# Kernel tuning notes

Measured on AMD Instinct MI355X. Metric: run time of the kernel, lower is better.

The kernel has to match this reference:

```python
import jax, jax.numpy as jnp
import numpy as np
import math

B = 256      # graphs per batch
NPG = 400    # nodes per graph (initial)
DEG = 16     # avg degree
F_IN = 128
H = 128
C = 2
NL = 5       # num_layers
RATIO = 0.8


def setup_inputs() -> dict:
    key = jax.random.key(0)
    ks = jax.random.split(key, 12)
    N = B * NPG
    E = B * NPG * DEG
    x = jax.random.normal(ks[0], (N, F_IN), dtype=jnp.float32)
    gid = jnp.repeat(jnp.arange(B, dtype=jnp.int32), NPG * DEG)
    src = jax.random.randint(ks[1], (E,), 0, NPG, dtype=jnp.int32) + gid * NPG
    dst = jax.random.randint(ks[2], (E,), 0, NPG, dtype=jnp.int32) + gid * NPG
    edge_index = jnp.stack([src, dst])
    batch = jnp.repeat(jnp.arange(B, dtype=jnp.int32), NPG)
    s = 0.05
    return dict(
        x=x, edge_index=edge_index, batch=batch,
        conv1_wr=jax.random.normal(ks[3], (F_IN, H), jnp.float32) * s,
        conv1_ws=jax.random.normal(ks[4], (F_IN, H), jnp.float32) * s,
        conv1_b=jnp.zeros((H,), jnp.float32),
        convs_wr=jax.random.normal(ks[5], (NL - 1, H, H), jnp.float32) * s,
        convs_ws=jax.random.normal(ks[6], (NL - 1, H, H), jnp.float32) * s,
        convs_b=jnp.zeros((NL - 1, H), jnp.float32),
        pools_wr=jax.random.normal(ks[7], ((NL - 1) // 2, H, 1), jnp.float32) * s,
        pools_ws=jax.random.normal(ks[8], ((NL - 1) // 2, H, 1), jnp.float32) * s,
        pools_b=jnp.zeros(((NL - 1) // 2, 1), jnp.float32),
        lin1_w=jax.random.normal(ks[9], (NL * H, H), jnp.float32) * s,
        lin1_b=jnp.zeros((H,), jnp.float32),
        lin2_w=jax.random.normal(ks[10], (H, C), jnp.float32) * s,
        lin2_b=jnp.zeros((C,), jnp.float32),
    )


def _graph_conv(x, src, dst, emask, n, wr, ws, b):
    # PyG GraphConv(aggr='mean'): mean_j(x_j) @ W_rel + x @ W_root + b
    msg = x[src] * emask[:, None]                       # [E, F]
    agg = jax.ops.segment_sum(msg, dst, num_segments=n)  # [N, F]
    cnt = jax.ops.segment_sum(emask, dst, num_segments=n)
    mean = agg / jnp.maximum(cnt, 1.0)[:, None]
    return mean @ wr + x @ ws + b


def _sag_pool(x, src, dst, emask, n, npg, wr, ws, b):
    # score via GraphConv(hidden, 1); per-graph top-k (fixed k since graphs equal-sized)
    score = _graph_conv(x, src, dst, emask, n, wr, ws, b)[:, 0]  # [N]
    nb = n // npg
    k = int(math.ceil(RATIO * npg))
    _, topi = jax.lax.top_k(score.reshape(nb, npg), k)           # [nb, k]
    perm = (topi + (jnp.arange(nb, dtype=topi.dtype) * npg)[:, None]).reshape(-1)
    new_x = x[perm] * jnp.tanh(score[perm])[:, None]
    # reindex edges; drop edges touching removed nodes via mask
    node_map = jnp.full((n,), -1, dtype=src.dtype).at[perm].set(
        jnp.arange(nb * k, dtype=src.dtype))
    ns, nd = node_map[src], node_map[dst]
    new_mask = emask * (ns >= 0).astype(emask.dtype) * (nd >= 0).astype(emask.dtype)
    return new_x, jnp.maximum(ns, 0), jnp.maximum(nd, 0), new_mask, nb * k, k


def reference(x, edge_index, batch, conv1_wr, conv1_ws, conv1_b,
              convs_wr, convs_ws, convs_b, pools_wr, pools_ws, pools_b,
              lin1_w, lin1_b, lin2_w, lin2_b):
    src, dst = edge_index[0], edge_index[1]
    emask = jnp.ones(src.shape, jnp.float32)
    n, npg = x.shape[0], NPG
    x = jax.nn.relu(_graph_conv(x, src, dst, emask, n, conv1_wr, conv1_ws, conv1_b))
    xs = [x.reshape(B, npg, H).mean(axis=1)]  # global_mean_pool (equal graph sizes)
    nconvs = NL - 1
    for i in range(nconvs):
        x = jax.nn.relu(_graph_conv(x, src, dst, emask, n,
                                    convs_wr[i], convs_ws[i], convs_b[i]))
        xs.append(x.reshape(B, npg, H).mean(axis=1))
        if i % 2 == 0 and i < nconvs - 1:
            j = i // 2
            x, src, dst, emask, n, npg = _sag_pool(
                x, src, dst, emask, n, npg, pools_wr[j], pools_ws[j], pools_b[j])
    h = jnp.concatenate(xs, axis=-1)            # JumpingKnowledge 'cat' -> [B, NL*H]
    h = jax.nn.relu(h @ lin1_w + lin1_b)        # dropout p=0.5 is identity (eval)
    logits = h @ lin2_w + lin2_b
    return jax.nn.log_softmax(logits, axis=-1)
```

## Files before the change

### kernel.cpp

```cpp
#include <hip/hip_runtime.h>
#include <math.h>

#define BGR 256
#define NPG0 400
#define NN (BGR*NPG0)
#define NE (NN*16)
#define HD 128
#define AST4 208
#define A32PG (NPG0*52)
#define KSA 13
#define MSTR 136
#define NTPB 5
#define SCGRID 2048
#define ACH4 1040

typedef __attribute__((ext_vector_type(8))) short short8;
typedef __attribute__((ext_vector_type(4))) float floatx4;
typedef __attribute__((ext_vector_type(4))) unsigned int uintx4;

__device__ __forceinline__ unsigned short f2b(float f) {
    unsigned int u = __builtin_bit_cast(unsigned int, f);
    unsigned int r = (u + 0x7fffu + ((u >> 16) & 1u)) >> 16;
    return (unsigned short)r;
}
__device__ __forceinline__ unsigned int pk2(float a, float b) {
    return (unsigned int)f2b(a) | ((unsigned int)f2b(b) << 16);
}
__device__ __forceinline__ float b2f_lo(unsigned int u) { return __builtin_bit_cast(float, u << 16); }
__device__ __forceinline__ float b2f_hi(unsigned int u) { return __builtin_bit_cast(float, u & 0xffff0000u); }
__device__ __forceinline__ short bfint(unsigned int v) {
    return (short)(__builtin_bit_cast(unsigned int, (float)v) >> 16);
}
__device__ __forceinline__ unsigned int pkb(short a, short b) {
    return (unsigned int)(unsigned short)a | ((unsigned int)(unsigned short)b << 16);
}
__device__ __forceinline__ short8 lutdec(unsigned int u, const unsigned int* lut) {
    uintx4 w;
    w[0] = lut[u & 0xFFu];
    w[1] = lut[(u >> 8) & 0xFFu];
    w[2] = lut[(u >> 16) & 0xFFu];
    w[3] = lut[u >> 24];
    return __builtin_bit_cast(short8, w);
}
__device__ __forceinline__ float nibdot(unsigned int u, const float* v) {
    return (float)(u & 0xFu) * v[0] + (float)((u >> 4) & 0xFu) * v[1]
         + (float)((u >> 8) & 0xFu) * v[2] + (float)((u >> 12) & 0xFu) * v[3]
         + (float)((u >> 16) & 0xFu) * v[4] + (float)((u >> 20) & 0xFu) * v[5]
         + (float)((u >> 24) & 0xFu) * v[6] + (float)(u >> 28) * v[7];
}

__global__ __launch_bounds__(512) void k_graph2(const int* __restrict__ src,
                                                const int* __restrict__ dst,
                                                unsigned int* __restrict__ A,
                                                float* __restrict__ alive,
                                                float* __restrict__ rliv) {
    __shared__ unsigned int sA[A32PG];
    int g = blockIdx.x, t = threadIdx.x;
    {
        uint4 z = {0u, 0u, 0u, 0u};
        uint4* s4 = (uint4*)sA;
        for (int i = t; i < A32PG / 4; i += 512) s4[i] = z;
    }
    __syncthreads();
    int ebase = g * (NPG0 * 16);
    int gb = g * NPG0;
    for (int i = t; i < NPG0 * 16; i += 512) {
        int s = src[ebase + i] - gb;
        int d = dst[ebase + i] - gb;
        int nib = d * 416 + s;
        atomicAdd(&sA[nib >> 3], 1u << ((nib & 7) * 4));
    }
    __syncthreads();
    {
        uint4* Ao = (uint4*)(A + (long)g * A32PG);
        const uint4* si = (const uint4*)sA;
        for (int i = t; i < A32PG / 4; i += 512) Ao[i] = si[i];
    }
    for (int n = t; n < NPG0; n += 512) {
        const unsigned int* row = &sA[n * 52];
        unsigned int deg = 0;
        for (int c = 0; c < 52; ++c) {
            unsigned int u = row[c];
            unsigned int p = (u & 0x0F0F0F0Fu) + ((u >> 4) & 0x0F0F0F0Fu);
            deg += (p * 0x01010101u) >> 24;
        }
        alive[gb + n] = 1.0f;
        rliv[gb + n] = 1.0f / fmaxf((float)deg, 1.0f);
    }
}

__global__ void k_wcvt(const float* __restrict__ c1_wr, const float* __restrict__ c1_ws,
                       const float* __restrict__ cs_wr, const float* __restrict__ cs_ws,
                       unsigned short* __restrict__ bt) {
    int m = blockIdx.y;
    int idx = blockIdx.x * 256 + threadIdx.x;
    const float* W = (m == 0) ? c1_wr : (m == 1) ? c1_ws
                   : (m < 6) ? (cs_wr + (m - 2) * HD * HD) : (cs_ws + (m - 6) * HD * HD);
    int n = idx >> 7, k = idx & 127;
    bt[m * HD * HD + idx] = f2b(W[k * HD + n]);
}

__global__ __launch_bounds__(512) void k_xt0(const float* __restrict__ xin,
                                             unsigned short* __restrict__ xt) {
    int t = threadIdx.x;
    int ngrp = blockIdx.x * 128 + (t >> 2);
    int j = t & 3;
    int r0 = ngrp * 4;
    int f0 = blockIdx.y * 4;
    float4 v = ((const float4*)xin)[(long)(r0 + j) * 32 + (f0 >> 2)];
    float a0 = v.x, a1 = v.y, a2 = v.z, a3 = v.w;
    float tw;
    bool bo1 = j & 1;
    tw = __shfl_xor(bo1 ? a0 : a1, 1); if (bo1) a0 = tw; else a1 = tw;
    tw = __shfl_xor(bo1 ? a2 : a3, 1); if (bo1) a2 = tw; else a3 = tw;
    bool bo2 = (j & 2) != 0;
    tw = __shfl_xor(bo2 ? a0 : a2, 2); if (bo2) a0 = tw; else a2 = tw;
    tw = __shfl_xor(bo2 ? a1 : a3, 2); if (bo2) a1 = tw; else a3 = tw;
    uint2 w; w.x = pk2(a0, a1); w.y = pk2(a2, a3);
    *(uint2*)&xt[(long)(f0 + j) * NN + r0] = w;
}

__global__ __launch_bounds__(256) void k_scale(unsigned short* __restrict__ xt,
                                               const float* __restrict__ multg)
{
    int tid = blockIdx.x * 256 + threadIdx.x;
    const int step = SCGRID * 256;
    for (int i = tid; i < HD * (NN / 4); i += step) {
        int f = i / (NN / 4), c = i - f * (NN / 4);
        int n4 = c * 4;
        unsigned short* p = &xt[(long)f * NN + n4];
        uint2 u = *(uint2*)p, w;
        w.x = pk2(b2f_lo(u.x) * multg[n4], b2f_hi(u.x) * multg[n4 + 1]);
        w.y = pk2(b2f_lo(u.y) * multg[n4 + 2], b2f_hi(u.y) * multg[n4 + 3]);
        *(uint2*)p = w;
    }
}

template<bool HASD, bool LAST>
__global__ __launch_bounds__(256, 3) void k_layer10(
    const unsigned short* __restrict__ xtin, unsigned short* __restrict__ xtout,
    const unsigned char* __restrict__ Amat,
    const float* __restrict__ alive, const float* __restrict__ rliv,
    const unsigned short* __restrict__ wr_bt, const unsigned short* __restrict__ ws_bt,
    const float* __restrict__ bias, float* __restrict__ hcat, int layer,
    const float* __restrict__ pwr, const float* __restrict__ pws, float* __restrict__ dd)
{
    __shared__ __align__(16) unsigned char sAM[NTPB * 16 * MSTR * 2];
    __shared__ __align__(16) unsigned short sX[NTPB * 16 * MSTR];
    __shared__ unsigned int sLUT[256];
    int g = blockIdx.x;
    int ntg = blockIdx.y;
    int t = threadIdx.x;
    long gbase = (long)g * NPG0;
    int lane = t & 63, wid = t >> 6;
    int quad = lane >> 4, l15 = lane & 15;
    int mp = wid;
    int nbase = ntg * (NTPB * 16);
    int gi = t >> 2, j4 = t & 3;

    sLUT[t] = pkb(bfint(t & 0xFu), bfint(t >> 4));

    const unsigned char* Ag = Amat + (gbase + nbase) * (long)AST4;
    uint4 astg[5];
    {
        const uint4* Ag4 = (const uint4*)Ag;
#pragma unroll
        for (int r = 0; r < 5; ++r) {
            int c = t + r * 256;
            if (c < ACH4) astg[r] = Ag4[c];
        }
    }
    uint2 stg[10];
#pragma unroll
    for (int it = 0; it < 10; ++it) {
        int tid2 = gi + it * 64;
        int fg = tid2 / 20, ng = tid2 - fg * 20;
        stg[it] = *(const uint2*)&xtin[(long)(fg * 4 + j4) * NN + gbase + nbase + ng * 4];
    }
    float rl[NTPB];
#pragma unroll
    for (int nt = 0; nt < NTPB; ++nt) rl[nt] = rliv[gbase + nbase + nt * 16 + l15];

#pragma unroll
    for (int r = 0; r < 5; ++r) {
        int c = t + r * 256;
        if (c < ACH4) *(uint4*)&sAM[c * 16] = astg[r];
    }
#pragma unroll
    for (int it = 0; it < 10; ++it) {
        int tid2 = gi + it * 64;
        int fg = tid2 / 20, ng = tid2 - fg * 20;
        uint2 u = stg[it];
        float a0 = b2f_lo(u.x), a1 = b2f_hi(u.x), a2 = b2f_lo(u.y), a3 = b2f_hi(u.y);
        float tw;
        bool bo1 = j4 & 1;
        tw = __shfl_xor(bo1 ? a0 : a1, 1); if (bo1) a0 = tw; else a1 = tw;
        tw = __shfl_xor(bo1 ? a2 : a3, 1); if (bo1) a2 = tw; else a3 = tw;
        bool bo2 = (j4 & 2) != 0;
        tw = __shfl_xor(bo2 ? a0 : a2, 2); if (bo2) a0 = tw; else a2 = tw;
        tw = __shfl_xor(bo2 ? a1 : a3, 2); if (bo2) a1 = tw; else a3 = tw;
        uint2 w; w.x = pk2(a0, a1); w.y = pk2(a2, a3);
        *(uint2*)&sX[(ng * 4 + j4) * MSTR + fg * 4] = w;
    }

    const unsigned short* xa0 = xtin + (long)(mp * 32 + l15) * NN + gbase;
    const unsigned short* xa1 = xa0 + (long)16 * NN;
    short8 Ac0 = *(const short8*)&xa0[quad * 8];
    short8 Ac1 = *(const short8*)&xa1[quad * 8];
    short8 An0 = *(const short8*)&xa0[32 + quad * 8];
    short8 An1 = *(const short8*)&xa1[32 + quad * 8];

    __syncthreads();

    floatx4 acc[NTPB][2];
#pragma unroll
    for (int nt = 0; nt < NTPB; ++nt) {
        acc[nt][0] = (floatx4){0.f, 0.f, 0.f, 0.f};
        acc[nt][1] = (floatx4){0.f, 0.f, 0.f, 0.f};
    }
    int abase = l15 * AST4 + quad * 4;
#pragma unroll
    for (int k = 0; k < KSA; ++k) {
        short8 Af0, Af1;
        if (k + 2 < KSA) {
            int ko = (k + 2) * 32 + quad * 8;
            Af0 = *(const short8*)&xa0[ko];
            Af1 = *(const short8*)&xa1[ko];
        }
#pragma unroll
        for (int nt = 0; nt < NTPB; ++nt) {
            unsigned int u = *(const unsigned int*)&sAM[abase + nt * (16 * AST4) + k * 16];
            short8 Bf = lutdec(u, sLUT);
            acc[nt][0] = __builtin_amdgcn_mfma_f32_16x16x32_bf16(Ac0, Bf, acc[nt][0], 0, 0, 0);
            acc[nt][1] = __builtin_amdgcn_mfma_f32_16x16x32_bf16(Ac1, Bf, acc[nt][1], 0, 0, 0);
        }
        if (k + 1 < KSA) { Ac0 = An0; Ac1 = An1; }
        if (k + 2 < KSA) { An0 = Af0; An1 = Af1; }
    }
    __syncthreads();

    unsigned short* sM = (unsigned short*)sAM;
#pragma unroll
    for (int nt = 0; nt < NTPB; ++nt) {
        int lo = nt * 16 + l15;
        unsigned short* mrow = &sM[lo * MSTR + 32 * mp + quad * 4];
        uint2 w0, w1;
        w0.x = pk2(acc[nt][0][0] * rl[nt], acc[nt][0][1] * rl[nt]);
        w0.y = pk2(acc[nt][0][2] * rl[nt], acc[nt][0][3] * rl[nt]);
        w1.x = pk2(acc[nt][1][0] * rl[nt], acc[nt][1][1] * rl[nt]);
        w1.y = pk2(acc[nt][1][2] * rl[nt], acc[nt][1][3] * rl[nt]);
        *(uint2*)mrow = w0;
        *(uint2*)(mrow + 16) = w1;
    }

    short8 Wr8[2][4], Ws8[2][4];
#pragma unroll
    for (int mt = 0; mt < 2; ++mt) {
        int jj = (2 * mp + mt) * 16 + l15;
#pragma unroll
        for (int k = 0; k < 4; ++k) {
            Wr8[mt][k] = *(const short8*)&wr_bt[jj * HD + k * 32 + quad * 8];
            Ws8[mt][k] = *(const short8*)&ws_bt[jj * HD + k * 32 + quad * 8];
        }
    }
    float4 b40 = *(const float4*)&bias[(2 * mp) * 16 + quad * 4];
    float4 b41 = *(const float4*)&bias[(2 * mp + 1) * 16 + quad * 4];
    float av[NTPB];
#pragma unroll
    for (int nt = 0; nt < NTPB; ++nt) av[nt] = alive[gbase + nbase + nt * 16 + l15];

    float4 pwrA, pwrB, pwsA, pwsB;
    if (HASD) {
        pwrA = *(const float4*)&pwr[(2 * mp) * 16 + quad * 4];
        pwrB = *(const float4*)&pwr[(2 * mp + 1) * 16 + quad * 4];
        pwsA = *(const float4*)&pws[(2 * mp) * 16 + quad * 4];
        pwsB = *(const float4*)&pws[(2 * mp + 1) * 16 + quad * 4];
    }
    __syncthreads();

    float ps0[4] = {0, 0, 0, 0}, ps1[4] = {0, 0, 0, 0};

#pragma unroll
    for (int nt = 0; nt < NTPB; ++nt) {
        int lo = nt * 16 + l15;
        long go = gbase + nbase + lo;
        floatx4 a0 = {b40.x, b40.y, b40.z, b40.w};
        floatx4 a1 = {b41.x, b41.y, b41.z, b41.w};
#pragma unroll
        for (int k = 0; k < 4; ++k) {
            short8 B0 = *(const short8*)&sM[lo * MSTR + k * 32 + quad * 8];
            a0 = __builtin_amdgcn_mfma_f32_16x16x32_bf16(Wr8[0][k], B0, a0, 0, 0, 0);
            a1 = __builtin_amdgcn_mfma_f32_16x16x32_bf16(Wr8[1][k], B0, a1, 0, 0, 0);
        }
#pragma unroll
        for (int k = 0; k < 4; ++k) {
            short8 B1 = *(const short8*)&sX[lo * MSTR + k * 32 + quad * 8];
            a0 = __builtin_amdgcn_mfma_f32_16x16x32_bf16(Ws8[0][k], B1, a0, 0, 0, 0);
            a1 = __builtin_amdgcn_mfma_f32_16x16x32_bf16(Ws8[1][k], B1, a1, 0, 0, 0);
        }
        bool liv = av[nt] != 0.0f;
        float v0r[4], v1r[4];
#pragma unroll
        for (int rr = 0; rr < 4; ++rr) {
            v0r[rr] = fmaxf(a0[rr], 0.0f);
            v1r[rr] = fmaxf(a1[rr], 0.0f);
            if (liv) { ps0[rr] += v0r[rr]; ps1[rr] += v1r[rr]; }
            if (!liv) { v0r[rr] = 0.0f; v1r[rr] = 0.0f; }
        }
        if (!LAST) {
#pragma unroll
            for (int rr = 0; rr < 4; ++rr) {
                xtout[(long)(32 * mp + quad * 4 + rr) * NN + go] = f2b(v0r[rr]);
                xtout[(long)(32 * mp + 16 + quad * 4 + rr) * NN + go] = f2b(v1r[rr]);
            }
        }
        if (HASD) {
            float pr = v0r[0]*pwrA.x + v0r[1]*pwrA.y + v0r[2]*pwrA.z + v0r[3]*pwrA.w
                     + v1r[0]*pwrB.x + v1r[1]*pwrB.y + v1r[2]*pwrB.z + v1r[3]*pwrB.w;
            float pd = v0r[0]*pwsA.x + v0r[1]*pwsA.y + v0r[2]*pwsA.z + v0r[3]*pwsA.w
                     + v1r[0]*pwsB.x + v1r[1]*pwsB.y + v1r[2]*pwsB.z + v1r[3]*pwsB.w;
            pr += __shfl_xor(pr, 16); pr += __shfl_xor(pr, 32);
            pd += __shfl_xor(pd, 16); pd += __shfl_xor(pd, 32);
            if (quad == 0) {
                float2 st = {pr, pd};
                *(float2*)&dd[go * 8 + mp * 2] = st;
            }
        }
    }
#pragma unroll
    for (int rr = 0; rr < 4; ++rr) {
        float v = ps0[rr];
        v += __shfl_xor(v, 1); v += __shfl_xor(v, 2); v += __shfl_xor(v, 4); v += __shfl_xor(v, 8);
        float u = ps1[rr];
        u += __shfl_xor(u, 1); u += __shfl_xor(u, 2); u += __shfl_xor(u, 4); u += __shfl_xor(u, 8);
        if (l15 == 0) {
            atomicAdd(&hcat[g * (5 * HD) + layer * HD + (2 * mp) * 16 + quad * 4 + rr], v);
            atomicAdd(&hcat[g * (5 * HD) + layer * HD + (2 * mp + 1) * 16 + quad * 4 + rr], u);
        }
    }
}

__global__ __launch_bounds__(512) void k_pool2(
    const float* __restrict__ dd, const unsigned int* __restrict__ A,
    float* __restrict__ multg, float* __restrict__ alive, float* __restrict__ rliv,
    const float* __restrict__ pb, int K)
{
    __shared__ float str[NPG0];
    __shared__ float stsb[NPG0];
    __shared__ float sal[NPG0];
    __shared__ float s[512];
    __shared__ float sc[NPG0];
    __shared__ float kf[NPG0];
    __shared__ unsigned char keep[NPG0];
    __shared__ unsigned int tmsk[13];
    __shared__ int cnt_gt;
    int g = blockIdx.x, t = threadIdx.x;
    long nb = (long)g * NPG0;
    float pbv = pb[0];

    for (int n = t; n < NPG0; n += 512) {
        const float* dp = &dd[(nb + n) * 8];
        float4 da = *(const float4*)dp;
        float4 db = *(const float4*)(dp + 4);
        str[n] = da.x + da.z + db.x + db.z;
        stsb[n] = da.y + da.w + db.y + db.w + pbv;
        sal[n] = alive[nb + n];
    }
    if (t == 0) cnt_gt = 0;
    if (t < 13) tmsk[t] = 0u;
    __syncthreads();

    for (int n = t; n < 512; n += 512) {
        float v = -INFINITY;
        if (n < NPG0 && sal[n] != 0.0f) {
            const uint4* Ar = (const uint4*)(A + ((long)g * NPG0 + n) * 52);
            float ssum = 0.0f;
#pragma unroll
            for (int c = 0; c < 13; ++c) {
                uint4 q = Ar[c];
                ssum += nibdot(q.x, &str[c * 32]);
                ssum += nibdot(q.y, &str[c * 32 + 8]);
                ssum += nibdot(q.z, &str[c * 32 + 16]);
                ssum += nibdot(q.w, &str[c * 32 + 24]);
            }
            v = ssum * rliv[nb + n] + stsb[n];
        }
        s[n] = v;
        if (n < NPG0) sc[n] = v;
    }
    __syncthreads();

    for (int ksz = 2; ksz <= 512; ksz <<= 1) {
        for (int jsz = ksz >> 1; jsz >= 1; jsz >>= 1) {
            for (int i = t; i < 512; i += 512) {
                int ixj = i ^ jsz;
                if (ixj > i) {
                    float a = s[i], c = s[ixj];
                    bool up = ((i & ksz) == 0);
                    if ((a > c) == up) { s[i] = c; s[ixj] = a; }
                }
            }
            __syncthreads();
        }
    }
    float thr = s[512 - K];
    for (int n = t; n < NPG0; n += 512) {
        if (sc[n] > thr) atomicAdd(&cnt_gt, 1);
        else if (sc[n] == thr) atomicOr(&tmsk[n >> 5], 1u << (n & 31));
    }
    __syncthreads();
    int m = K - cnt_gt;
    for (int n = t; n < NPG0; n += 512) {
        bool kp = sc[n] > thr;
        if (!kp && sc[n] == thr) {
            int w = n >> 5;
            int rank = __popc(tmsk[w] & ((1u << (n & 31)) - 1u));
            for (int j = 0; j < w; ++j) rank += __popc(tmsk[j]);
            kp = rank < m;
        }
        keep[n] = kp ? 1 : 0;
    }
    __syncthreads();
    for (int n = t; n < NPG0; n += 512) {
        multg[nb + n] = keep[n] ? tanhf(sc[n]) : 0.0f;
        alive[nb + n] = keep[n] ? 1.0f : 0.0f;
        kf[n] = keep[n] ? 1.0f : 0.0f;
    }
    __syncthreads();
    for (int n = t; n < NPG0; n += 512) {
        const uint4* Ar = (const uint4*)(A + ((long)g * NPG0 + n) * 52);
        float ssum = 0.0f;
#pragma unroll
        for (int c = 0; c < 13; ++c) {
            uint4 q = Ar[c];
            ssum += nibdot(q.x, &kf[c * 32]);
            ssum += nibdot(q.y, &kf[c * 32 + 8]);
            ssum += nibdot(q.z, &kf[c * 32 + 16]);
            ssum += nibdot(q.w, &kf[c * 32 + 24]);
        }
        rliv[nb + n] = 1.0f / fmaxf(ssum, 1.0f);
    }
}

__global__ __launch_bounds__(128) void k_mlp(const float* __restrict__ h, const float* __restrict__ w1,
    const float* __restrict__ b1, const float* __restrict__ w2,
    const float* __restrict__ b2, float* __restrict__ out) {
    __shared__ float h1[HD];
    __shared__ float red[HD];
    __shared__ float lg[2];
    const float inv[5] = {1.0f/400.0f, 1.0f/400.0f, 1.0f/320.0f, 1.0f/320.0f, 1.0f/256.0f};
    int g = blockIdx.x, j = threadIdx.x;
    const float* hg = &h[g * (5 * HD)];
    float acc = b1[j];
    for (int k = 0; k < 5 * HD; k++) acc += hg[k] * inv[k >> 7] * w1[k * HD + j];
    h1[j] = fmaxf(acc, 0.0f);
    __syncthreads();
    for (int c = 0; c < 2; c++) {
        red[j] = h1[j] * w2[j * 2 + c];
        __syncthreads();
        for (int st = 64; st > 0; st >>= 1) {
            if (j < st) red[j] += red[j + st];
            __syncthreads();
        }
        if (j == 0) lg[c] = red[0] + b2[c];
        __syncthreads();
    }
    if (j == 0) {
        float l0 = lg[0], l1 = lg[1];
        float m = fmaxf(l0, l1);
        float lse = m + logf(expf(l0 - m) + expf(l1 - m));
        out[g * 2 + 0] = l0 - lse;
        out[g * 2 + 1] = l1 - lse;
    }
}

extern "C" void kernel_launch(void* const* d_in, const int* in_sizes, int n_in,
                              void* d_out, int out_size, void* d_ws, size_t ws_size,
                              hipStream_t stream) {
    const float* x_in   = (const float*)d_in[0];
    const int*   eidx   = (const int*)d_in[1];
    const int*   e_src  = eidx;
    const int*   e_dst  = eidx + NE;
    const float* c1_wr  = (const float*)d_in[3];
    const float* c1_ws  = (const float*)d_in[4];
    const float* c1_b   = (const float*)d_in[5];
    const float* cs_wr  = (const float*)d_in[6];
    const float* cs_ws  = (const float*)d_in[7];
    const float* cs_b   = (const float*)d_in[8];
    const float* p_wr   = (const float*)d_in[9];
    const float* p_ws   = (const float*)d_in[10];
    const float* p_b    = (const float*)d_in[11];
    const float* l1_w   = (const float*)d_in[12];
    const float* l1_b   = (const float*)d_in[13];
    const float* l2_w   = (const float*)d_in[14];
    const float* l2_b   = (const float*)d_in[15];
    float* out = (float*)d_out;

    char* ws = (char*)d_ws;
    size_t off = 0;
    float* alive = (float*)(ws + off);           off += (size_t)NN * 4;
    float* rliv  = (float*)(ws + off);           off += (size_t)NN * 4;
    float* hcat  = (float*)(ws + off);           off += (size_t)BGR * 5 * HD * 4;
    unsigned short* wbt = (unsigned short*)(ws + off); off += (size_t)10 * HD * HD * 2;
    unsigned int* Amat = (unsigned int*)(ws + off);    off += (size_t)NN * 52 * 4;
    unsigned short* xtA = (unsigned short*)(ws + off); off += ((size_t)NN * HD + 32) * 2;
    unsigned short* xtB = (unsigned short*)(ws + off); off += ((size_t)NN * HD + 32) * 2;
    float* dd    = (float*)(ws + off);           off += (size_t)NN * 8 * 4;
    float* multg = (float*)(ws + off);           off += (size_t)NN * 4;

    hipMemsetAsync(hcat, 0, (size_t)BGR * 5 * HD * 4, stream);
    hipMemsetAsync(xtA + (size_t)NN * HD, 0, 64, stream);
    hipMemsetAsync(xtB + (size_t)NN * HD, 0, 64, stream);

    k_graph2<<<BGR, 512, 0, stream>>>(e_src, e_dst, Amat, alive, rliv);
    k_wcvt<<<dim3(64, 10), 256, 0, stream>>>(c1_wr, c1_ws, cs_wr, cs_ws, wbt);
    k_xt0<<<dim3(200, 32), 512, 0, stream>>>(x_in, xtB);

    unsigned short* bt_wr[5] = { wbt + 0 * HD * HD, wbt + 2 * HD * HD, wbt + 3 * HD * HD, wbt + 4 * HD * HD, wbt + 5 * HD * HD };
    unsigned short* bt_ws[5] = { wbt + 1 * HD * HD, wbt + 6 * HD * HD, wbt + 7 * HD * HD, wbt + 8 * HD * HD, wbt + 9 * HD * HD };
    const unsigned char* Am8 = (const unsigned char*)Amat;

    k_layer10<false, false><<<dim3(BGR, NTPB), 256, 0, stream>>>(
        xtB, xtA, Am8, alive, rliv,
        bt_wr[0], bt_ws[0], c1_b, hcat, 0, nullptr, nullptr, nullptr);
    k_layer10<true, false><<<dim3(BGR, NTPB), 256, 0, stream>>>(
        xtA, xtB, Am8, alive, rliv,
        bt_wr[1], bt_ws[1], cs_b + 0 * HD, hcat, 1, p_wr + 0 * HD, p_ws + 0 * HD, dd);
    k_pool2<<<BGR, 512, 0, stream>>>(dd, Amat, multg, alive, rliv, p_b + 0, 320);
    k_scale<<<SCGRID, 256, 0, stream>>>(xtB, multg);
    k_layer10<false, false><<<dim3(BGR, NTPB), 256, 0, stream>>>(
        xtB, xtA, Am8, alive, rliv,
        bt_wr[2], bt_ws[2], cs_b + 1 * HD, hcat, 2, nullptr, nullptr, nullptr);
    k_layer10<true, false><<<dim3(BGR, NTPB), 256, 0, stream>>>(
        xtA, xtB, Am8, alive, rliv,
        bt_wr[3], bt_ws[3], cs_b + 2 * HD, hcat, 3, p_wr + 1 * HD, p_ws + 1 * HD, dd);
    k_pool2<<<BGR, 512, 0, stream>>>(dd, Amat, multg, alive, rliv, p_b + 1, 256);
    k_scale<<<SCGRID, 256, 0, stream>>>(xtB, multg);
    k_layer10<false, true><<<dim3(BGR, NTPB), 256, 0, stream>>>(
        xtB, nullptr, Am8, alive, rliv,
        bt_wr[4], bt_ws[4], cs_b + 3 * HD, hcat, 4, nullptr, nullptr, nullptr);
    k_mlp<<<BGR, HD, 0, stream>>>(hcat, l1_w, l1_b, l2_w, l2_b, out);
}
```

Baseline: 512.5 us.

## Tile transposed feature buffer into per-graph 16-node blocks

Changes the bf16 transposed feature buffer from a feature-major [HD][NN] layout to a tiled layout of 25 tiles per graph, each holding 128 features by 16 nodes. The producer, the scale kernel, the layer kernel's staging loads, its MFMA A-operand loads and its output stores are all rewritten for the new indexing. The aim is to make each block's global reads and writes contiguous, instead of strided by NN per feature row, which should cut wasted DRAM and cache traffic. The output stores of 16 consecutive lanes now land in one contiguous row. Padding at the end of each buffer grows to one tile.

Result: faster. 467.0 us (-8.9%).

```diff
diff --git a/kernel.cpp b/kernel.cpp
--- a/kernel.cpp
+++ b/kernel.cpp
@@ -13,6 +13,9 @@
 #define NTPB 5
 #define SCGRID 2048
 #define ACH4 1040
+#define TPG 25
+#define TSTR 2048
+#define GSTR (TPG*TSTR)
 
 typedef __attribute__((ext_vector_type(8))) short short8;
 typedef __attribute__((ext_vector_type(4))) float floatx4;
@@ -117,7 +120,10 @@
     tw = __shfl_xor(bo2 ? a0 : a2, 2); if (bo2) a0 = tw; else a2 = tw;
     tw = __shfl_xor(bo2 ? a1 : a3, 2); if (bo2) a1 = tw; else a3 = tw;
     uint2 w; w.x = pk2(a0, a1); w.y = pk2(a2, a3);
-    *(uint2*)&xt[(long)(f0 + j) * NN + r0] = w;
+    int g = r0 / NPG0;
+    int ln = r0 - g * NPG0;
+    int tl = ln >> 4, n0 = ln & 15;
+    *(uint2*)&xt[((long)(g * TPG + tl) * HD + f0 + j) * 16 + n0] = w;
 }
 
 __global__ __launch_bounds__(256) void k_scale(unsigned short* __restrict__ xt,
@@ -125,19 +131,24 @@
 {
     int tid = blockIdx.x * 256 + threadIdx.x;
     const int step = SCGRID * 256;
-    for (int i = tid; i < HD * (NN / 4); i += step) {
-        int f = i / (NN / 4), c = i - f * (NN / 4);
-        int n4 = c * 4;
-        unsigned short* p = &xt[(long)f * NN + n4];
+    const int total = BGR * TPG * 512;
+    for (int i = tid; i < total; i += step) {
+        int gt = i >> 9;
+        int rem = i & 511;
+        int f = rem >> 2;
+        int n0 = (rem & 3) * 4;
+        int g = gt / TPG, tl = gt - g * TPG;
+        int nb = g * NPG0 + tl * 16 + n0;
+        unsigned short* p = &xt[(long)gt * TSTR + f * 16 + n0];
         uint2 u = *(uint2*)p, w;
-        w.x = pk2(b2f_lo(u.x) * multg[n4], b2f_hi(u.x) * multg[n4 + 1]);
-        w.y = pk2(b2f_lo(u.y) * multg[n4 + 2], b2f_hi(u.y) * multg[n4 + 3]);
+        w.x = pk2(b2f_lo(u.x) * multg[nb], b2f_hi(u.x) * multg[nb + 1]);
+        w.y = pk2(b2f_lo(u.y) * multg[nb + 2], b2f_hi(u.y) * multg[nb + 3]);
         *(uint2*)p = w;
     }
 }
 
 template<bool HASD, bool LAST>
-__global__ __launch_bounds__(256, 3) void k_layer10(
+__global__ __launch_bounds__(256, 3) void k_layer14(
     const unsigned short* __restrict__ xtin, unsigned short* __restrict__ xtout,
     const unsigned char* __restrict__ Amat,
     const float* __restrict__ alive, const float* __restrict__ rliv,
@@ -170,12 +181,16 @@
             if (c < ACH4) astg[r] = Ag4[c];
         }
     }
+    long gt0 = (long)(g * TPG + ntg * NTPB);
     uint2 stg[10];
 #pragma unroll
     for (int it = 0; it < 10; ++it) {
         int tid2 = gi + it * 64;
-        int fg = tid2 / 20, ng = tid2 - fg * 20;
-        stg[it] = *(const uint2*)&xtin[(long)(fg * 4 + j4) * NN + gbase + nbase + ng * 4];
+        int tl = tid2 >> 7;
+        int rem = tid2 & 127;
+        int fg = rem >> 2;
+        int ng = rem & 3;
+        stg[it] = *(const uint2*)&xtin[((gt0 + tl) * HD + fg * 4 + j4) * 16 + ng * 4];
     }
     float rl[NTPB];
 #pragma unroll
@@ -189,7 +204,10 @@
 #pragma unroll
     for (int it = 0; it < 10; ++it) {
         int tid2 = gi + it * 64;
-        int fg = tid2 / 20, ng = tid2 - fg * 20;
+        int tl = tid2 >> 7;
+        int rem = tid2 & 127;
+        int fg = rem >> 2;
+        int ng = rem & 3;
         uint2 u = stg[it];
         float a0 = b2f_lo(u.x), a1 = b2f_hi(u.x), a2 = b2f_lo(u.y), a3 = b2f_hi(u.y);
         float tw;
@@ -200,15 +218,17 @@
         tw = __shfl_xor(bo2 ? a0 : a2, 2); if (bo2) a0 = tw; else a2 = tw;
         tw = __shfl_xor(bo2 ? a1 : a3, 2); if (bo2) a1 = tw; else a3 = tw;
         uint2 w; w.x = pk2(a0, a1); w.y = pk2(a2, a3);
-        *(uint2*)&sX[(ng * 4 + j4) * MSTR + fg * 4] = w;
-    }
-
-    const unsigned short* xa0 = xtin + (long)(mp * 32 + l15) * NN + gbase;
-    const unsigned short* xa1 = xa0 + (long)16 * NN;
-    short8 Ac0 = *(const short8*)&xa0[quad * 8];
-    short8 Ac1 = *(const short8*)&xa1[quad * 8];
-    short8 An0 = *(const short8*)&xa0[32 + quad * 8];
-    short8 An1 = *(const short8*)&xa1[32 + quad * 8];
+        *(uint2*)&sX[(tl * 16 + ng * 4 + j4) * MSTR + fg * 4] = w;
+    }
+
+    const unsigned short* Xg = xtin + (long)g * GSTR;
+    int qhi = quad >> 1, qlo = (quad & 1) * 8;
+    const unsigned short* xb0 = Xg + (long)qhi * TSTR + (mp * 32 + l15) * 16 + qlo;
+    const unsigned short* xb1 = xb0 + 16 * 16;
+    short8 Ac0 = *(const short8*)&xb0[0];
+    short8 Ac1 = *(const short8*)&xb1[0];
+    short8 An0 = *(const short8*)&xb0[2 * TSTR];
+    short8 An1 = *(const short8*)&xb1[2 * TSTR];
 
     __syncthreads();
 
@@ -223,9 +243,8 @@
     for (int k = 0; k < KSA; ++k) {
         short8 Af0, Af1;
         if (k + 2 < KSA) {
-            int ko = (k + 2) * 32 + quad * 8;
-            Af0 = *(const short8*)&xa0[ko];
-            Af1 = *(const short8*)&xa1[ko];
+            Af0 = *(const short8*)&xb0[(k + 2) * 2 * TSTR];
+            Af1 = *(const short8*)&xb1[(k + 2) * 2 * TSTR];
         }
 #pragma unroll
         for (int nt = 0; nt < NTPB; ++nt) {
@@ -308,10 +327,11 @@
             if (!liv) { v0r[rr] = 0.0f; v1r[rr] = 0.0f; }
         }
         if (!LAST) {
+            unsigned short* orow = &xtout[(gt0 + nt) * TSTR];
 #pragma unroll
             for (int rr = 0; rr < 4; ++rr) {
-                xtout[(long)(32 * mp + quad * 4 + rr) * NN + go] = f2b(v0r[rr]);
-                xtout[(long)(32 * mp + 16 + quad * 4 + rr) * NN + go] = f2b(v1r[rr]);
+                orow[((2 * mp) * 16 + quad * 4 + rr) * 16 + l15] = f2b(v0r[rr]);
+                orow[((2 * mp + 1) * 16 + quad * 4 + rr) * 16 + l15] = f2b(v1r[rr]);
             }
         }
         if (HASD) {
@@ -503,14 +523,14 @@
     float* hcat  = (float*)(ws + off);           off += (size_t)BGR * 5 * HD * 4;
     unsigned short* wbt = (unsigned short*)(ws + off); off += (size_t)10 * HD * HD * 2;
     unsigned int* Amat = (unsigned int*)(ws + off);    off += (size_t)NN * 52 * 4;
-    unsigned short* xtA = (unsigned short*)(ws + off); off += ((size_t)NN * HD + 32) * 2;
-    unsigned short* xtB = (unsigned short*)(ws + off); off += ((size_t)NN * HD + 32) * 2;
+    unsigned short* xtA = (unsigned short*)(ws + off); off += ((size_t)BGR * GSTR + TSTR) * 2;
+    unsigned short* xtB = (unsigned short*)(ws + off); off += ((size_t)BGR * GSTR + TSTR) * 2;
     float* dd    = (float*)(ws + off);           off += (size_t)NN * 8 * 4;
     float* multg = (float*)(ws + off);           off += (size_t)NN * 4;
 
     hipMemsetAsync(hcat, 0, (size_t)BGR * 5 * HD * 4, stream);
-    hipMemsetAsync(xtA + (size_t)NN * HD, 0, 64, stream);
-    hipMemsetAsync(xtB + (size_t)NN * HD, 0, 64, stream);
+    hipMemsetAsync(xtA + (size_t)BGR * GSTR, 0, TSTR * 2, stream);
+    hipMemsetAsync(xtB + (size_t)BGR * GSTR, 0, TSTR * 2, stream);
 
     k_graph2<<<BGR, 512, 0, stream>>>(e_src, e_dst, Amat, alive, rliv);
     k_wcvt<<<dim3(64, 10), 256, 0, stream>>>(c1_wr, c1_ws, cs_wr, cs_ws, wbt);
@@ -520,23 +540,23 @@
     unsigned short* bt_ws[5] = { wbt + 1 * HD * HD, wbt + 6 * HD * HD, wbt + 7 * HD * HD, wbt + 8 * HD * HD, wbt + 9 * HD * HD };
     const unsigned char* Am8 = (const unsigned char*)Amat;
 
-    k_layer10<false, false><<<dim3(BGR, NTPB), 256, 0, stream>>>(
+    k_layer14<false, false><<<dim3(BGR, NTPB), 256, 0, stream>>>(
         xtB, xtA, Am8, alive, rliv,
         bt_wr[0], bt_ws[0], c1_b, hcat, 0, nullptr, nullptr, nullptr);
-    k_layer10<true, false><<<dim3(BGR, NTPB), 256, 0, stream>>>(
+    k_layer14<true, false><<<dim3(BGR, NTPB), 256, 0, stream>>>(
         xtA, xtB, Am8, alive, rliv,
         bt_wr[1], bt_ws[1], cs_b + 0 * HD, hcat, 1, p_wr + 0 * HD, p_ws + 0 * HD, dd);
     k_pool2<<<BGR, 512, 0, stream>>>(dd, Amat, multg, alive, rliv, p_b + 0, 320);
     k_scale<<<SCGRID, 256, 0, stream>>>(xtB, multg);
-    k_layer10<false, false><<<dim3(BGR, NTPB), 256, 0, stream>>>(
+    k_layer14<false, false><<<dim3(BGR, NTPB), 256, 0, stream>>>(
         xtB, xtA, Am8, alive, rliv,
         bt_wr[2], bt_ws[2], cs_b + 1 * HD, hcat, 2, nullptr, nullptr, nullptr);
-    k_layer10<true, false><<<dim3(BGR, NTPB), 256, 0, stream>>>(
+    k_layer14<true, false><<<dim3(BGR, NTPB), 256, 0, stream>>>(
         xtA, xtB, Am8, alive, rliv,
         bt_wr[3], bt_ws[3], cs_b + 2 * HD, hcat, 3, p_wr + 1 * HD, p_ws + 1 * HD, dd);
     k_pool2<<<BGR, 512, 0, stream>>>(dd, Amat, multg, alive, rliv, p_b + 1, 256);
     k_scale<<<SCGRID, 256, 0, stream>>>(xtB, multg);
-    k_layer10<false, true><<<dim3(BGR, NTPB), 256, 0, stream>>>(
+    k_layer14<false, true><<<dim3(BGR, NTPB), 256, 0, stream>>>(
         xtB, nullptr, Am8, alive, rliv,
         bt_wr[4], bt_ws[4], cs_b + 3 * HD, hcat, 4, nullptr, nullptr, nullptr);
     k_mlp<<<BGR, HD, 0, stream>>>(hcat, l1_w, l1_b, l2_w, l2_b, out);
```
